# Kernel optimization log

Hardware: AMD Instinct MI355X
Metric: run time of the kernel (lower is better)

## Reference

```python
import jax, jax.numpy as jnp
import numpy as np

N = 200000   # points in scene batch
M = 32       # backbone feature width (cfg.m)
P = 64       # proposals after clustering
D = 16       # self.output_dim
NUM_PARAMS = (D + 3) * D + D + D + 1  # 337 = weight_nums + bias_nums


def _bn(x, g, b, eps=1e-5):
    # BatchNorm1d, training-mode batch stats over the point/instance axis
    mu = x.mean(axis=0)
    var = x.var(axis=0)
    return (x - mu) * jax.lax.rsqrt(var + eps) * g + b


def setup_inputs() -> dict:
    key = jax.random.key(0)
    ks = jax.random.split(key, 16)
    s = 0.1
    return {
        "feats": jax.random.normal(ks[0], (N, M), jnp.float32),
        "coords": jax.random.normal(ks[1], (N, 3), jnp.float32),
        "inst_feats": jax.random.normal(ks[2], (P, M), jnp.float32),
        "centers": jax.random.normal(ks[3], (P, 3), jnp.float32),
        "mask_w1": jax.random.normal(ks[4], (M, M), jnp.float32) * s,
        "mask_g1": jnp.ones((M,), jnp.float32), "mask_b1": jnp.zeros((M,), jnp.float32),
        "mask_w2": jax.random.normal(ks[5], (M, M), jnp.float32) * s,
        "mask_g2": jnp.ones((M,), jnp.float32), "mask_b2": jnp.zeros((M,), jnp.float32),
        "mask_w3": jax.random.normal(ks[6], (M, M), jnp.float32) * s,
        "mask_g3": jnp.ones((M,), jnp.float32), "mask_b3": jnp.zeros((M,), jnp.float32),
        "mask_w_out": jax.random.normal(ks[7], (M, D), jnp.float32) * s,
        "mask_b_out": jnp.zeros((D,), jnp.float32),
        # before_embedding_tower: conv1d 1x1 m->16 no-bias, BN, ReLU
        "emb_w": jax.random.normal(ks[8], (M, D), jnp.float32) * s,
        "emb_g": jnp.ones((D,), jnp.float32), "emb_b": jnp.zeros((D,), jnp.float32),
        # controller: conv1d 1x1 16->337 (std=0.01 init, zero bias)
        "ctrl_w": jax.random.normal(ks[9], (D, NUM_PARAMS), jnp.float32) * 0.01,
        "ctrl_b": jnp.zeros((NUM_PARAMS,), jnp.float32),
    }


def reference(feats, coords, inst_feats, centers,
              mask_w1, mask_g1, mask_b1,
              mask_w2, mask_g2, mask_b2,
              mask_w3, mask_g3, mask_b3,
              mask_w_out, mask_b_out,
              emb_w, emb_g, emb_b,
              ctrl_w, ctrl_b):
    # --- mask tower: per-point 1x1 convs ---
    x = feats
    for w, g, b in ((mask_w1, mask_g1, mask_b1),
                    (mask_w2, mask_g2, mask_b2),
                    (mask_w3, mask_g3, mask_b3)):
        x = jax.nn.relu(_bn(x @ w, g, b))
    mask_feats = x @ mask_w_out + mask_b_out                      # [N, D]

    # --- controller: generate dynamic filters per proposal ---
    e = jax.nn.relu(_bn(inst_feats @ emb_w, emb_g, emb_b))        # [P, D]
    params = e @ ctrl_w + ctrl_b                                  # [P, 337]
    w1 = params[:, :(D + 3) * D].reshape(P, D, D + 3)             # [P, out=16, in=19]
    w2 = params[:, (D + 3) * D:(D + 3) * D + D]                   # [P, 16] (out=1)
    b1 = params[:, (D + 4) * D:(D + 4) * D + D]                   # [P, 16]
    b2 = params[:, (D + 4) * D + D:]                              # [P, 1]

    # --- dynamic conv over all points; input = [rel_coords(3) | mask_feats(16)] ---
    rel = coords[None, :, :] - centers[:, None, :]                # [P, N, 3]
    h = (jnp.einsum('pnc,pdc->pnd', rel, w1[:, :, :3])
         + jnp.einsum('nc,pdc->pnd', mask_feats, w1[:, :, 3:])
         + b1[:, None, :])                                        # [P, N, 16]
    h = jax.nn.relu(h)
    logits = jnp.einsum('pnd,pd->pn', h, w2) + b2                 # [P, N]
    return logits
```

## Files before the change

kernel.cpp:

```cpp
#include <hip/hip_runtime.h>
#include <hip/hip_bf16.h>
#include <math.h>

#define N_PTS 200000
#define M 32
#define P_INST 64
#define D 16
#define NP 337

#define NBL ((N_PTS + 255) / 256)
#define HPB 128
#define NBH ((N_PTS + HPB - 1) / HPB)

#define WS_PARAMS 0
#define WS_STATS  21568
#define WS_W2     21760
#define WS_B2     22784
#define WS_APACK  22912
#define WS_Y      104832

typedef __attribute__((ext_vector_type(8))) short short8v;
typedef __attribute__((ext_vector_type(4))) float floatx4;

static __device__ __forceinline__ unsigned short f2bf(float v) {
    __hip_bfloat16 h = __float2bfloat16(v);
    return *reinterpret_cast<unsigned short*>(&h);
}

__global__ __launch_bounds__(1024) void k_prep(
    const float* __restrict__ inst, const float* __restrict__ emb_w,
    const float* __restrict__ emb_g, const float* __restrict__ emb_b,
    const float* __restrict__ ctrl_w, const float* __restrict__ ctrl_b,
    const float* __restrict__ centers,
    float* __restrict__ params, float* __restrict__ apackf,
    float* __restrict__ w2p, float* __restrict__ b2p)
{
    __shared__ float sInst[P_INST * M];
    __shared__ float sCW[D * NP];
    __shared__ float sE[P_INST * D];
    __shared__ float sA[D], sC[D];
    int t = threadIdx.x;
    int lane = t & 63, wv = t >> 6;

    for (int i = t; i < P_INST * M; i += 1024) sInst[i] = inst[i];
    for (int i = t; i < D * NP; i += 1024) sCW[i] = ctrl_w[i];
    __syncthreads();

    {
        int p = t >> 4, d = t & (D - 1);
        float acc = 0.f;
        #pragma unroll
        for (int k = 0; k < M; k++) acc = fmaf(sInst[p * M + k], emb_w[k * D + d], acc);
        sE[t] = acc;
    }
    __syncthreads();

    if (t < D) {
        float s = 0.f, q = 0.f;
        for (int p = 0; p < P_INST; p++) { float v = sE[p * D + t]; s += v; q += v * v; }
        float mu = s * (1.f / P_INST);
        float var = q * (1.f / P_INST) - mu * mu;
        float a = emb_g[t] * rsqrtf(var + 1e-5f);
        sA[t] = a;
        sC[t] = emb_b[t] - mu * a;
    }
    __syncthreads();

    {
        int d = t & (D - 1);
        sE[t] = fmaxf(sE[t] * sA[d] + sC[d], 0.f);
    }
    __syncthreads();

    #pragma unroll
    for (int pp = 0; pp < 4; pp++) {
        int p = wv * 4 + pp;
        float e[D];
        #pragma unroll
        for (int d = 0; d < D; d++) e[d] = sE[p * D + d];
        for (int q = lane; q < NP; q += 64) {
            float acc = ctrl_b[q];
            #pragma unroll
            for (int d = 0; d < D; d++) acc = fmaf(e[d], sCW[d * NP + q], acc);
            params[p * NP + q] = acc;
        }
    }
    __threadfence_block();
    __syncthreads();

    int row = lane & 15, kbase = (lane >> 4) * 8;
    #pragma unroll
    for (int pi = 0; pi < 4; pi++) {
        int p = wv + pi * 16;
        const float* pp = params + p * NP;
        unsigned int w[4];
        #pragma unroll
        for (int i = 0; i < 4; i++) {
            unsigned short lo = 0, hi = 0;
            #pragma unroll
            for (int h = 0; h < 2; h++) {
                int k = kbase + 2 * i + h;
                float v;
                if (k < 19) v = pp[row * 19 + k];
                else if (k == 19)
                    v = pp[320 + row] - (centers[p * 3 + 0] * pp[row * 19 + 0]
                                       + centers[p * 3 + 1] * pp[row * 19 + 1]
                                       + centers[p * 3 + 2] * pp[row * 19 + 2]);
                else v = 0.f;
                if (h == 0) lo = f2bf(v); else hi = f2bf(v);
            }
            w[i] = (unsigned)lo | ((unsigned)hi << 16);
        }
        uint4* dst = (uint4*)((char*)apackf + (size_t)p * 1024 + lane * 16);
        *dst = make_uint4(w[0], w[1], w[2], w[3]);

        if (lane < 16) w2p[p * 16 + lane] = pp[304 + lane];
        if (lane == 0) b2p[p] = pp[336];
    }
}

template <int L>
__global__ __launch_bounds__(256) void k_layer(
    const float* __restrict__ feats, const float* __restrict__ W,
    const float* __restrict__ stats, float* __restrict__ ybuf,
    float* __restrict__ partials)
{
    __shared__ float tr[256 * 33];
    __shared__ float red2[2][8][32];
    int t = threadIdx.x;
    int n = blockIdx.x * 256 + t;
    bool valid = n < N_PTS;
    int nc = valid ? n : N_PTS - 1;

    const float* src = ((L == 0) ? feats : ybuf) + (size_t)nc * M;
    float x[M];
    #pragma unroll
    for (int q = 0; q < M / 4; q++) {
        float4 v = ((const float4*)src)[q];
        x[4*q] = v.x; x[4*q+1] = v.y; x[4*q+2] = v.z; x[4*q+3] = v.w;
    }
    if (L > 0) {
        const float* st = stats + (L - 1) * 64;
        #pragma unroll
        for (int j = 0; j < M; j++) x[j] = fmaxf(fmaf(x[j], st[j], st[32 + j]), 0.f);
    }
    float y[M];
    #pragma unroll
    for (int j = 0; j < M; j++) y[j] = 0.f;
    #pragma unroll
    for (int i = 0; i < M; i++) {
        float xi = x[i];
        #pragma unroll
        for (int j = 0; j < M; j++) y[j] = fmaf(xi, W[i * M + j], y[j]);
    }
    if (valid) {
        float4* dst = (float4*)(ybuf + (size_t)n * M);
        #pragma unroll
        for (int q = 0; q < M / 4; q++)
            dst[q] = make_float4(y[4*q], y[4*q+1], y[4*q+2], y[4*q+3]);
    } else {
        #pragma unroll
        for (int j = 0; j < M; j++) y[j] = 0.f;
    }

    #pragma unroll
    for (int j = 0; j < M; j++) tr[t * 33 + j] = y[j];
    __syncthreads();
    int c = t & 31, s = t >> 5;
    float S = 0.f, Q = 0.f;
    #pragma unroll
    for (int r = 0; r < 32; r++) {
        float v = tr[(s * 32 + r) * 33 + c];
        S += v; Q += v * v;
    }
    red2[0][s][c] = S;
    red2[1][s][c] = Q;
    __syncthreads();
    if (t < 64) {
        int cc = t & 31, k = t >> 5;
        float a = 0.f;
        #pragma unroll
        for (int sl = 0; sl < 8; sl++) a += red2[k][sl][cc];
        partials[(size_t)blockIdx.x * 64 + k * 32 + cc] = a;
    }
}

__global__ __launch_bounds__(256) void k_reduce(
    const float* __restrict__ partials,
    const float* __restrict__ g, const float* __restrict__ b,
    float* __restrict__ stats_out)
{
    int c = blockIdx.x;
    int t = threadIdx.x;
    int part = t >> 7;
    int i0 = t & 127;
    float s = 0.f;
    for (int i = i0; i < NBL; i += 128)
        s += partials[(size_t)i * 64 + part * 32 + c];
    __shared__ float sh[256];
    sh[t] = s;
    __syncthreads();
    #pragma unroll
    for (int off = 64; off; off >>= 1) {
        if ((t & 127) < off) sh[t] += sh[t + off];
        __syncthreads();
    }
    if (t == 0) {
        float S = sh[0], Q = sh[128];
        float mu = S * (1.f / N_PTS);
        float var = Q * (1.f / N_PTS) - mu * mu;
        float a = g[c] * rsqrtf(var + 1e-5f);
        stats_out[c] = a;
        stats_out[32 + c] = b[c] - mu * a;
    }
}

__global__ __launch_bounds__(512, 2) void k_head(
    const float* __restrict__ ybuf, const float* __restrict__ coords,
    const float* __restrict__ w_out, const float* __restrict__ b_out,
    const float* __restrict__ stats, const float* __restrict__ w2p,
    const float* __restrict__ b2p, const float* __restrict__ apackf,
    float* __restrict__ out)
{
    __shared__ unsigned int zlds[HPB * 20];
    unsigned short* zlds16 = (unsigned short*)zlds;
    int t = threadIdx.x;
    int nblk = blockIdx.x * HPB;

    {
        int pt = t & 127, qd = t >> 7;
        int nc = nblk + pt;
        if (nc >= N_PTS) nc = N_PTS - 1;
        const float* yr = ybuf + (size_t)nc * M;
        float x[M];
        #pragma unroll
        for (int q = 0; q < M / 4; q++) {
            float4 v = ((const float4*)yr)[q];
            x[4*q] = v.x; x[4*q+1] = v.y; x[4*q+2] = v.z; x[4*q+3] = v.w;
        }
        const float* st = stats + 128;
        #pragma unroll
        for (int j = 0; j < M; j++) x[j] = fmaxf(fmaf(x[j], st[j], st[32 + j]), 0.f);

        float mf[4];
        #pragma unroll
        for (int d = 0; d < 4; d++) mf[d] = b_out[qd * 4 + d];
        #pragma unroll
        for (int i = 0; i < M; i++) {
            float xi = x[i];
            #pragma unroll
            for (int d = 0; d < 4; d++) mf[d] = fmaf(xi, w_out[i * D + qd * 4 + d], mf[d]);
        }
        unsigned short* zp = zlds16 + pt * 40;
        #pragma unroll
        for (int d = 0; d < 4; d++) zp[3 + qd * 4 + d] = f2bf(mf[d]);
        if (qd == 0) {
            zp[0] = f2bf(coords[(size_t)nc * 3 + 0]);
            zp[1] = f2bf(coords[(size_t)nc * 3 + 1]);
            zp[2] = f2bf(coords[(size_t)nc * 3 + 2]);
            zp[19] = 0x3F80;
        } else if (qd == 3) {
            unsigned int* zw = (unsigned int*)(zp + 20);
            #pragma unroll
            for (int i = 0; i < 10; i++) zw[i] = 0u;
        }
    }
    __syncthreads();

    int lane = t & 63, wv = t >> 6;
    int slab = wv & 1, pq = wv >> 1;
    int cl = lane & 15, kg = lane >> 4;
    int n0 = nblk + slab * 64;
    int nn = n0 + lane;
    bool wr = nn < N_PTS;

    short8v b8[4];
    #pragma unroll
    for (int s = 0; s < 4; s++)
        b8[s] = *(const short8v*)&zlds[(slab * 64 + s * 16 + cl) * 20 + kg * 4];

    const char* abase = (const char*)apackf + (size_t)(pq * 16) * 1024 + lane * 16;
    float* outb = out + (size_t)(pq * 16) * N_PTS + nn;

    short8v a8n = *(const short8v*)abase;

    #pragma unroll 4
    for (int i = 0; i < 16; i++) {
        int p = pq * 16 + i;
        short8v a8 = a8n;
        if (i < 15) a8n = *(const short8v*)(abase + (size_t)(i + 1) * 1024);
        floatx4 w2v = *(const floatx4*)(w2p + p * 16 + kg * 4);
        float b2 = b2p[p];

        float vs[4];
        #pragma unroll
        for (int s = 0; s < 4; s++) {
            floatx4 acc = {0.f, 0.f, 0.f, 0.f};
            acc = __builtin_amdgcn_mfma_f32_16x16x32_bf16(a8, b8[s], acc, 0, 0, 0);
            float m01 = fmaxf(acc[0], 0.f) * w2v[0];
            m01 = fmaf(fmaxf(acc[1], 0.f), w2v[1], m01);
            float m23 = fmaxf(acc[2], 0.f) * w2v[2];
            m23 = fmaf(fmaxf(acc[3], 0.f), w2v[3], m23);
            float v = m01 + m23;
            v += __shfl_xor(v, 16, 64);
            v += __shfl_xor(v, 32, 64);
            vs[s] = v;
        }
        float vout = (kg == 0) ? vs[0] : (kg == 1) ? vs[1] : (kg == 2) ? vs[2] : vs[3];
        if (wr) outb[(size_t)i * N_PTS] = vout + b2;
    }
}

extern "C" void kernel_launch(void* const* d_in, const int* in_sizes, int n_in,
                              void* d_out, int out_size, void* d_ws, size_t ws_size,
                              hipStream_t stream) {
    const float* feats   = (const float*)d_in[0];
    const float* coords  = (const float*)d_in[1];
    const float* inst    = (const float*)d_in[2];
    const float* centers = (const float*)d_in[3];
    const float* mw1 = (const float*)d_in[4];
    const float* mg1 = (const float*)d_in[5];
    const float* mb1 = (const float*)d_in[6];
    const float* mw2 = (const float*)d_in[7];
    const float* mg2 = (const float*)d_in[8];
    const float* mb2 = (const float*)d_in[9];
    const float* mw3 = (const float*)d_in[10];
    const float* mg3 = (const float*)d_in[11];
    const float* mb3 = (const float*)d_in[12];
    const float* wout = (const float*)d_in[13];
    const float* bout = (const float*)d_in[14];
    const float* embw = (const float*)d_in[15];
    const float* embg = (const float*)d_in[16];
    const float* embb = (const float*)d_in[17];
    const float* cw   = (const float*)d_in[18];
    const float* cb   = (const float*)d_in[19];

    float* wsf      = (float*)d_ws;
    float* params   = wsf + WS_PARAMS;
    float* stats    = wsf + WS_STATS;
    float* w2p      = wsf + WS_W2;
    float* b2p      = wsf + WS_B2;
    float* apackf   = wsf + WS_APACK;
    float* ybuf     = wsf + WS_Y;
    float* out      = (float*)d_out;
    float* partials = (float*)d_out;

    k_prep<<<1, 1024, 0, stream>>>(inst, embw, embg, embb, cw, cb, centers,
                                   params, apackf, w2p, b2p);

    k_layer<0><<<NBL, 256, 0, stream>>>(feats, mw1, stats, ybuf, partials);
    k_reduce<<<32, 256, 0, stream>>>(partials, mg1, mb1, stats + 0);

    k_layer<1><<<NBL, 256, 0, stream>>>(feats, mw2, stats, ybuf, partials);
    k_reduce<<<32, 256, 0, stream>>>(partials, mg2, mb2, stats + 64);

    k_layer<2><<<NBL, 256, 0, stream>>>(feats, mw3, stats, ybuf, partials);
    k_reduce<<<32, 256, 0, stream>>>(partials, mg3, mb3, stats + 128);

    k_head<<<NBH, 512, 0, stream>>>(ybuf, coords, wout, bout, stats,
                                    w2p, b2p, apackf, out);
}
```

Before: 158.8 us.

## Switch head dynamic-conv to 32x32x16 MFMA with two proposals per tile

The head kernel's per-proposal dynamic conv moves from four 16x16x32 MFMAs per proposal to 32x32x16 MFMAs. Each tile packs two proposals' 16 output channels into 32 rows, and the K dimension is split into two chunks. The prep kernel repacks the A operands to match. w2 and b2 are staged in LDS in the accumulator-register order, which cuts cross-lane shuffles and per-iteration global loads. The mask-feature projection is now done by 128 threads each computing all 16 outputs, and the occupancy hint changes to waves_per_eu(2,4). The cost is more MFMA FLOPs spent on K padding and higher register pressure.

```diff
diff --git a/kernel.cpp b/kernel.cpp
--- a/kernel.cpp
+++ b/kernel.cpp
@@ -21,6 +21,7 @@
 
 typedef __attribute__((ext_vector_type(8))) short short8v;
 typedef __attribute__((ext_vector_type(4))) float floatx4;
+typedef __attribute__((ext_vector_type(16))) float floatx16;
 
 static __device__ __forceinline__ unsigned short f2bf(float v) {
     __hip_bfloat16 h = __float2bfloat16(v);
@@ -88,34 +89,51 @@
     __threadfence_block();
     __syncthreads();
 
-    int row = lane & 15, kbase = (lane >> 4) * 8;
-    #pragma unroll
-    for (int pi = 0; pi < 4; pi++) {
-        int p = wv + pi * 16;
-        const float* pp = params + p * NP;
-        unsigned int w[4];
-        #pragma unroll
-        for (int i = 0; i < 4; i++) {
-            unsigned short lo = 0, hi = 0;
+    {
+        int row = lane & 31;
+        int d = row & 15, psub = row >> 4;
+        #pragma unroll
+        for (int half = 0; half < 2; half++) {
+            int pp = wv + half * 16;
+            int p = pp * 2 + psub;
+            const float* prm = params + p * NP;
+            float bias = prm[320 + d] - (centers[p * 3 + 0] * prm[d * 19 + 0]
+                                       + centers[p * 3 + 1] * prm[d * 19 + 1]
+                                       + centers[p * 3 + 2] * prm[d * 19 + 2]);
             #pragma unroll
-            for (int h = 0; h < 2; h++) {
-                int k = kbase + 2 * i + h;
-                float v;
-                if (k < 19) v = pp[row * 19 + k];
-                else if (k == 19)
-                    v = pp[320 + row] - (centers[p * 3 + 0] * pp[row * 19 + 0]
-                                       + centers[p * 3 + 1] * pp[row * 19 + 1]
-                                       + centers[p * 3 + 2] * pp[row * 19 + 2]);
-                else v = 0.f;
-                if (h == 0) lo = f2bf(v); else hi = f2bf(v);
+            for (int kc = 0; kc < 2; kc++) {
+                int kbase = kc * 16 + (lane >> 5) * 8;
+                unsigned int w[4];
+                #pragma unroll
+                for (int i = 0; i < 4; i++) {
+                    unsigned short lo = 0, hi = 0;
+                    #pragma unroll
+                    for (int h = 0; h < 2; h++) {
+                        int k = kbase + 2 * i + h;
+                        float v;
+                        if (k < 19) v = prm[d * 19 + k];
+                        else if (k == 19) v = bias;
+                        else v = 0.f;
+                        if (h == 0) lo = f2bf(v); else hi = f2bf(v);
+                    }
+                    w[i] = (unsigned)lo | ((unsigned)hi << 16);
+                }
+                uint4* dst = (uint4*)((char*)apackf + (size_t)pp * 2048
+                                      + kc * 1024 + lane * 16);
+                *dst = make_uint4(w[0], w[1], w[2], w[3]);
             }
-            w[i] = (unsigned)lo | ((unsigned)hi << 16);
-        }
-        uint4* dst = (uint4*)((char*)apackf + (size_t)p * 1024 + lane * 16);
-        *dst = make_uint4(w[0], w[1], w[2], w[3]);
-
-        if (lane < 16) w2p[p * 16 + lane] = pp[304 + lane];
-        if (lane == 0) b2p[p] = pp[336];
+        }
+    }
+
+    {
+        int row = lane & 15, dummy = row; (void)dummy;
+        #pragma unroll
+        for (int pi = 0; pi < 4; pi++) {
+            int p = wv + pi * 16;
+            const float* prm = params + p * NP;
+            if (lane < 16) w2p[p * 16 + lane] = prm[304 + lane];
+            if (lane == 0) b2p[p] = prm[336];
+        }
     }
 }
 
@@ -215,7 +233,9 @@
     }
 }
 
-__global__ __launch_bounds__(512, 2) void k_head(
+__global__ __launch_bounds__(512)
+__attribute__((amdgpu_waves_per_eu(2, 4)))
+void k_head(
     const float* __restrict__ ybuf, const float* __restrict__ coords,
     const float* __restrict__ w_out, const float* __restrict__ b_out,
     const float* __restrict__ stats, const float* __restrict__ w2p,
@@ -223,13 +243,13 @@
     float* __restrict__ out)
 {
     __shared__ unsigned int zlds[HPB * 20];
-    unsigned short* zlds16 = (unsigned short*)zlds;
+    __shared__ float w2lds[32 * 32];
+    __shared__ float b2lds[64];
     int t = threadIdx.x;
     int nblk = blockIdx.x * HPB;
 
-    {
-        int pt = t & 127, qd = t >> 7;
-        int nc = nblk + pt;
+    if (t < HPB) {
+        int nc = nblk + t;
         if (nc >= N_PTS) nc = N_PTS - 1;
         const float* yr = ybuf + (size_t)nc * M;
         float x[M];
@@ -242,72 +262,100 @@
         #pragma unroll
         for (int j = 0; j < M; j++) x[j] = fmaxf(fmaf(x[j], st[j], st[32 + j]), 0.f);
 
-        float mf[4];
-        #pragma unroll
-        for (int d = 0; d < 4; d++) mf[d] = b_out[qd * 4 + d];
+        float mf[D];
+        #pragma unroll
+        for (int d = 0; d < D; d++) mf[d] = b_out[d];
         #pragma unroll
         for (int i = 0; i < M; i++) {
             float xi = x[i];
             #pragma unroll
-            for (int d = 0; d < 4; d++) mf[d] = fmaf(xi, w_out[i * D + qd * 4 + d], mf[d]);
-        }
-        unsigned short* zp = zlds16 + pt * 40;
-        #pragma unroll
-        for (int d = 0; d < 4; d++) zp[3 + qd * 4 + d] = f2bf(mf[d]);
-        if (qd == 0) {
-            zp[0] = f2bf(coords[(size_t)nc * 3 + 0]);
-            zp[1] = f2bf(coords[(size_t)nc * 3 + 1]);
-            zp[2] = f2bf(coords[(size_t)nc * 3 + 2]);
-            zp[19] = 0x3F80;
-        } else if (qd == 3) {
-            unsigned int* zw = (unsigned int*)(zp + 20);
-            #pragma unroll
-            for (int i = 0; i < 10; i++) zw[i] = 0u;
+            for (int d = 0; d < D; d++) mf[d] = fmaf(xi, w_out[i * D + d], mf[d]);
+        }
+        float z[20];
+        z[0] = coords[(size_t)nc * 3 + 0];
+        z[1] = coords[(size_t)nc * 3 + 1];
+        z[2] = coords[(size_t)nc * 3 + 2];
+        #pragma unroll
+        for (int d = 0; d < D; d++) z[3 + d] = mf[d];
+        z[19] = 1.0f;
+
+        unsigned int zw[16];
+        #pragma unroll
+        for (int i = 0; i < 10; i++)
+            zw[i] = (unsigned)f2bf(z[2 * i]) | ((unsigned)f2bf(z[2 * i + 1]) << 16);
+        #pragma unroll
+        for (int i = 10; i < 16; i++) zw[i] = 0u;
+        uint4* zd = (uint4*)&zlds[t * 20];
+        #pragma unroll
+        for (int i = 0; i < 4; i++)
+            zd[i] = make_uint4(zw[4*i], zw[4*i+1], zw[4*i+2], zw[4*i+3]);
+    } else if (t < 256) {
+        int t2 = t - 128;
+        if (t2 < 64) b2lds[t2] = b2p[t2];
+        #pragma unroll
+        for (int e = 0; e < 8; e++) {
+            int idx = t2 * 8 + e;
+            int pp = idx >> 5;
+            int rem = idx & 31;
+            int hi = rem >> 4, reg = rem & 15;
+            int R = (reg & 3) + 8 * (reg >> 2) + 4 * hi;
+            int p = pp * 2 + (R >> 4), d = R & 15;
+            w2lds[idx] = w2p[p * 16 + d];
         }
     }
     __syncthreads();
 
     int lane = t & 63, wv = t >> 6;
-    int slab = wv & 1, pq = wv >> 1;
-    int cl = lane & 15, kg = lane >> 4;
-    int n0 = nblk + slab * 64;
-    int nn = n0 + lane;
+    int slab = wv & 3, ph = wv >> 2;
+    int col = lane & 31, hi = lane >> 5;
+    int n0 = nblk + slab * 32;
+    int nn = n0 + col;
     bool wr = nn < N_PTS;
 
-    short8v b8[4];
-    #pragma unroll
-    for (int s = 0; s < 4; s++)
-        b8[s] = *(const short8v*)&zlds[(slab * 64 + s * 16 + cl) * 20 + kg * 4];
-
-    const char* abase = (const char*)apackf + (size_t)(pq * 16) * 1024 + lane * 16;
-    float* outb = out + (size_t)(pq * 16) * N_PTS + nn;
-
-    short8v a8n = *(const short8v*)abase;
+    const unsigned int* zrow = &zlds[(slab * 32 + col) * 20];
+    short8v B1 = *(const short8v*)(zrow + hi * 4);
+    short8v B2 = *(const short8v*)(zrow + 8 + hi * 4);
+
+    const char* abase = (const char*)apackf + (size_t)(ph * 16) * 2048 + lane * 16;
 
     #pragma unroll 4
     for (int i = 0; i < 16; i++) {
-        int p = pq * 16 + i;
-        short8v a8 = a8n;
-        if (i < 15) a8n = *(const short8v*)(abase + (size_t)(i + 1) * 1024);
-        floatx4 w2v = *(const floatx4*)(w2p + p * 16 + kg * 4);
-        float b2 = b2p[p];
-
-        float vs[4];
-        #pragma unroll
-        for (int s = 0; s < 4; s++) {
-            floatx4 acc = {0.f, 0.f, 0.f, 0.f};
-            acc = __builtin_amdgcn_mfma_f32_16x16x32_bf16(a8, b8[s], acc, 0, 0, 0);
-            float m01 = fmaxf(acc[0], 0.f) * w2v[0];
-            m01 = fmaf(fmaxf(acc[1], 0.f), w2v[1], m01);
-            float m23 = fmaxf(acc[2], 0.f) * w2v[2];
-            m23 = fmaf(fmaxf(acc[3], 0.f), w2v[3], m23);
-            float v = m01 + m23;
-            v += __shfl_xor(v, 16, 64);
-            v += __shfl_xor(v, 32, 64);
-            vs[s] = v;
-        }
-        float vout = (kg == 0) ? vs[0] : (kg == 1) ? vs[1] : (kg == 2) ? vs[2] : vs[3];
-        if (wr) outb[(size_t)i * N_PTS] = vout + b2;
+        int pp = ph * 16 + i;
+        short8v A1 = *(const short8v*)(abase + (size_t)i * 2048);
+        short8v A2 = *(const short8v*)(abase + (size_t)i * 2048 + 1024);
+        const float* w2r = &w2lds[pp * 32 + hi * 16];
+        floatx4 w2a = *(const floatx4*)(w2r + 0);
+        floatx4 w2b = *(const floatx4*)(w2r + 4);
+        floatx4 w2c = *(const floatx4*)(w2r + 8);
+        floatx4 w2d = *(const floatx4*)(w2r + 12);
+        float b2 = b2lds[pp * 2 + hi];
+
+        floatx16 acc = {};
+        acc = __builtin_amdgcn_mfma_f32_32x32x16_bf16(A1, B1, acc, 0, 0, 0);
+        acc = __builtin_amdgcn_mfma_f32_32x32x16_bf16(A2, B2, acc, 0, 0, 0);
+
+        float pA = fmaxf(acc[0], 0.f) * w2a[0];
+        pA = fmaf(fmaxf(acc[1], 0.f), w2a[1], pA);
+        pA = fmaf(fmaxf(acc[2], 0.f), w2a[2], pA);
+        pA = fmaf(fmaxf(acc[3], 0.f), w2a[3], pA);
+        pA = fmaf(fmaxf(acc[4], 0.f), w2b[0], pA);
+        pA = fmaf(fmaxf(acc[5], 0.f), w2b[1], pA);
+        pA = fmaf(fmaxf(acc[6], 0.f), w2b[2], pA);
+        pA = fmaf(fmaxf(acc[7], 0.f), w2b[3], pA);
+        float pB = fmaxf(acc[8], 0.f) * w2c[0];
+        pB = fmaf(fmaxf(acc[9], 0.f), w2c[1], pB);
+        pB = fmaf(fmaxf(acc[10], 0.f), w2c[2], pB);
+        pB = fmaf(fmaxf(acc[11], 0.f), w2c[3], pB);
+        pB = fmaf(fmaxf(acc[12], 0.f), w2d[0], pB);
+        pB = fmaf(fmaxf(acc[13], 0.f), w2d[1], pB);
+        pB = fmaf(fmaxf(acc[14], 0.f), w2d[2], pB);
+        pB = fmaf(fmaxf(acc[15], 0.f), w2d[3], pB);
+
+        pA += __shfl_xor(pA, 32, 64);
+        pB += __shfl_xor(pB, 32, 64);
+
+        float vout = (hi ? pB : pA) + b2;
+        if (wr) out[(size_t)(pp * 2 + hi) * N_PTS + nn] = vout;
     }
 }
 
```

Measured after the change: 147.2 us. 7.3% less time.
